# Performance work log

Measured on AMD Instinct MI355X. Metric: run time of the kernel, lower is better.

The kernel has to match this reference:

```python
import jax, jax.numpy as jnp
import numpy as np

EMBED_DIM = 1024
NUM_HEADS = 16
HEAD_DIM = EMBED_DIM // NUM_HEADS  # 64
GRID_H, GRID_W = 24, 24
BASE = 10000.0


def rope2d_cache(head_dim=HEAD_DIM, grid_h=GRID_H, grid_w=GRID_W, base=BASE):
    # "Concatenated Embeddings" 2D RoPE cache -> (cos, sin), each [grid_h*grid_w, head_dim]
    pos_dim = head_dim // 2
    inv_freq = 1.0 / (base ** (jnp.arange(0, pos_dim, 2, dtype=jnp.float32) / pos_dim))
    max_grid = max(grid_h, grid_w)
    positions = jnp.arange(max_grid, dtype=jnp.float32)
    freqs = positions[:, None] * inv_freq[None, :]            # [max_grid, pos_dim//2]
    emb_1d = jnp.concatenate([freqs, freqs], axis=-1)          # [max_grid, pos_dim]
    h_emb = jnp.broadcast_to(emb_1d[:grid_h, None, :], (grid_h, grid_w, pos_dim))
    w_emb = jnp.broadcast_to(emb_1d[None, :grid_w, :], (grid_h, grid_w, pos_dim))
    emb_2d = jnp.concatenate([h_emb, w_emb], axis=-1).reshape(-1, head_dim)
    return jnp.cos(emb_2d), jnp.sin(emb_2d)


def rotate_half(x):
    x1, x2 = jnp.split(x, 2, axis=-1)
    return jnp.concatenate([-x2, x1], axis=-1)


def setup_inputs() -> dict:
    key = jax.random.key(0)
    ks = jax.random.split(key, 9)
    B, S, E = 16, GRID_H * GRID_W + 1, EMBED_DIM
    s = 1.0 / np.sqrt(E)
    inp = {
        "hidden_states": jax.random.normal(ks[0], (B, S, E), dtype=jnp.float32),
        "Wq": jax.random.normal(ks[1], (E, E), dtype=jnp.float32) * s,
        "bq": jnp.zeros((E,), dtype=jnp.float32),
        "Wk": jax.random.normal(ks[2], (E, E), dtype=jnp.float32) * s,
        "bk": jnp.zeros((E,), dtype=jnp.float32),
        "Wv": jax.random.normal(ks[3], (E, E), dtype=jnp.float32) * s,
        "bv": jnp.zeros((E,), dtype=jnp.float32),
        "Wo": jax.random.normal(ks[4], (E, E), dtype=jnp.float32) * s,
        "bo": jnp.zeros((E,), dtype=jnp.float32),
    }
    return inp


def reference(hidden_states, Wq, bq, Wk, bk, Wv, bv, Wo, bo):
    B, S, E = hidden_states.shape
    H, D = NUM_HEADS, HEAD_DIM
    scale = D ** -0.5

    def proj(W, b):
        # torch Linear: x @ W.T + b; reshape to [B, H, S, D]
        y = jnp.einsum('bse,fe->bsf', hidden_states, W) + b
        return y.reshape(B, S, H, D).transpose(0, 2, 1, 3)

    q = proj(Wq, bq)
    k = proj(Wk, bk)
    v = proj(Wv, bv)

    cos, sin = rope2d_cache()                 # [num_patches, D]
    cos = cos[None, None, :, :]
    sin = sin[None, None, :, :]

    # CLS token at position 0 is untouched; RoPE applied to patch tokens 1:
    qp = q[:, :, 1:, :]
    kp = k[:, :, 1:, :]
    qp = qp * cos + rotate_half(qp) * sin
    kp = kp * cos + rotate_half(kp) * sin
    q = jnp.concatenate([q[:, :, :1, :], qp], axis=2)
    k = jnp.concatenate([k[:, :, :1, :], kp], axis=2)

    scores = jnp.einsum('bhqd,bhkd->bhqk', q, k) * scale   # [B,H,S,S]
    attn = jax.nn.softmax(scores, axis=-1)
    out = jnp.einsum('bhqk,bhkd->bhqd', attn, v)           # [B,H,S,D]
    out = out.transpose(0, 2, 1, 3).reshape(B, S, E)
    out = jnp.einsum('bse,fe->bsf', out, Wo) + bo
    return out
```

## Files before the change

### kernel.cpp

```cpp
#include <hip/hip_runtime.h>
#include <hip/hip_bf16.h>
#include <stdint.h>

typedef __bf16 bf16_t;
typedef __attribute__((ext_vector_type(4))) float floatx4;
typedef __attribute__((ext_vector_type(8))) __bf16 bf16x8;
typedef __attribute__((ext_vector_type(4))) __bf16 bf16x4;

#define MFMA16(a, b, c) __builtin_amdgcn_mfma_f32_16x16x32_bf16(a, b, c, 0, 0, 0)

#define GLOAD_LDS16(gsrc, ldst)                                                          \
  __builtin_amdgcn_global_load_lds((const __attribute__((address_space(1))) void*)(gsrc),\
                                   (__attribute__((address_space(3))) void*)(ldst),      \
                                   16, 0, 0)

#define BATCH 16
#define SEQ   577
#define EMB   1024
#define NH    16
#define HD    64
#define SPAD  640
#define MROWS (BATCH * SEQ)
#define MPAD  9344

#define EXP_C 0.1803368801111404f

#define OFF_H  0ULL
#define OFF_WQ 19136512ULL
#define OFF_WK 21233664ULL
#define OFF_WV 23330816ULL
#define OFF_WO 25427968ULL
#define OFF_Q  27525120ULL
#define OFF_K  48496640ULL
#define OFF_VT 69468160ULL
#define OFF_AO 90439680ULL

__global__ __launch_bounds__(256) void k_cast(
    const float4* __restrict__ hs, const float4* __restrict__ wq,
    const float4* __restrict__ wk, const float4* __restrict__ wv,
    const float4* __restrict__ wo, bf16x4* __restrict__ hb, bf16x4* __restrict__ wqb,
    bf16x4* __restrict__ wkb, bf16x4* __restrict__ wvb, bf16x4* __restrict__ wob) {
  int idx = blockIdx.x * 256 + threadIdx.x;
  const int H4 = MROWS * EMB / 4;
  const int W4 = EMB * EMB / 4;
  const float4* src;
  bf16x4* dst;
  int i;
  if (idx < H4) {
    src = hs; dst = hb; i = idx;
  } else {
    int r = idx - H4;
    int w = r / W4;
    if (w >= 4) return;
    i = r - w * W4;
    src = (w == 0) ? wq : (w == 1) ? wk : (w == 2) ? wv : wo;
    dst = (w == 0) ? wqb : (w == 1) ? wkb : (w == 2) ? wvb : wob;
  }
  float4 v = src[i];
  bf16x4 o;
  o.x = (bf16_t)v.x; o.y = (bf16_t)v.y; o.z = (bf16_t)v.z; o.w = (bf16_t)v.w;
  dst[i] = o;
}

__global__ __launch_bounds__(256, 3) void k_qkv(const bf16_t* __restrict__ A,
                                                const bf16_t* __restrict__ Wq,
                                                const bf16_t* __restrict__ Wk,
                                                const bf16_t* __restrict__ Wv,
                                                const float* __restrict__ bq,
                                                const float* __restrict__ bk,
                                                const float* __restrict__ bv,
                                                bf16_t* __restrict__ qb,
                                                bf16_t* __restrict__ kb,
                                                bf16_t* __restrict__ vtb) {
  __shared__ bf16_t As[128 * 32];
  __shared__ bf16_t Bs[3 * 64 * 32];
  const int hh = blockIdx.x;
  const int n0 = hh * 64;
  const int m0 = blockIdx.y * 128;
  const int t = threadIdx.x;
  const int wid = t >> 6, lane = t & 63, quad = lane >> 4, c = lane & 15;

  floatx4 acc[3][2][4];
#pragma unroll
  for (int z = 0; z < 3; z++)
#pragma unroll
    for (int i = 0; i < 2; i++)
#pragma unroll
      for (int j = 0; j < 4; j++) {
        floatx4 zz = {0.f, 0.f, 0.f, 0.f};
        acc[z][i][j] = zz;
      }

  for (int k0 = 0; k0 < EMB; k0 += 32) {
    __syncthreads();
#pragma unroll
    for (int i = 0; i < 2; i++) {
      int ci = i * 256 + t;
      int row = ci >> 2, off = (ci & 3) * 8;
      GLOAD_LDS16(A + (size_t)(m0 + row) * EMB + k0 + off, (char*)As + (i * 256 + wid * 64) * 16);
    }
    {
      int row = t >> 2, off = (t & 3) * 8;
      GLOAD_LDS16(Wq + (size_t)(n0 + row) * EMB + k0 + off, (char*)Bs + (wid * 64) * 16);
      GLOAD_LDS16(Wk + (size_t)(n0 + row) * EMB + k0 + off, (char*)Bs + 4096 + (wid * 64) * 16);
      GLOAD_LDS16(Wv + (size_t)(n0 + row) * EMB + k0 + off, (char*)Bs + 8192 + (wid * 64) * 16);
    }
    __syncthreads();
    bf16x8 af[2];
#pragma unroll
    for (int mi = 0; mi < 2; mi++)
      af[mi] = *(const bf16x8*)(As + (wid * 32 + mi * 16 + c) * 32 + quad * 8);
#pragma unroll
    for (int z = 0; z < 3; z++) {
      bf16x8 bfr[4];
#pragma unroll
      for (int ni = 0; ni < 4; ni++)
        bfr[ni] = *(const bf16x8*)(Bs + z * 2048 + (ni * 16 + c) * 32 + quad * 8);
#pragma unroll
      for (int mi = 0; mi < 2; mi++)
#pragma unroll
        for (int ni = 0; ni < 4; ni++) acc[z][mi][ni] = MFMA16(af[mi], bfr[ni], acc[z][mi][ni]);
    }
  }

  const float invf = exp2f(-(float)c * 0.8304820237218405f);

  for (int z = 0; z < 3; z++) {
    const float* bias = (z == 0) ? bq : (z == 1) ? bk : bv;
    float bias_v[4];
#pragma unroll
    for (int ni = 0; ni < 4; ni++) bias_v[ni] = bias[n0 + ni * 16 + c];
#pragma unroll
    for (int mi = 0; mi < 2; mi++) {
#pragma unroll
      for (int r = 0; r < 4; r++) {
        int m = m0 + wid * 32 + mi * 16 + quad * 4 + r;
        if (m >= MROWS) continue;
        int bb = m / SEQ;
        int s = m - bb * SEQ;
        if (z < 2) {
          float ch = 1.f, sh = 0.f, cw = 1.f, sw = 0.f;
          if (s > 0) {
            int p = s - 1;
            int hp = p / 24, wp = p - (p / 24) * 24;
            __sincosf((float)hp * invf, &sh, &ch);
            __sincosf((float)wp * invf, &sw, &cw);
          }
          bf16_t* dst = (z == 0) ? qb : kb;
          size_t rowoff = ((size_t)(bb * NH + hh) * SPAD + s) * HD;
#pragma unroll
          for (int ni = 0; ni < 4; ni++) {
            float val = acc[z][mi][ni][r] + bias_v[ni];
            float part = acc[z][mi][ni ^ 2][r] + bias_v[ni ^ 2];
            float rot = (ni < 2) ? -part : part;
            float cs = (ni < 2) ? ch : cw;
            float sn = (ni < 2) ? sh : sw;
            dst[rowoff + ni * 16 + c] = (bf16_t)(val * cs + rot * sn);
          }
        } else {
          size_t base = (size_t)(bb * NH + hh) * HD;
#pragma unroll
          for (int ni = 0; ni < 4; ni++) {
            float val = acc[z][mi][ni][r] + bias_v[ni];
            int d = ni * 16 + c;
            vtb[(base + d) * SPAD + s] = (bf16_t)val;
          }
        }
      }
    }
  }
}

#define PSTR 72
#define OSTR 66
__global__ __launch_bounds__(256, 4) void k_attn(const bf16_t* __restrict__ qb,
                                                 const bf16_t* __restrict__ kb,
                                                 const bf16_t* __restrict__ vtb,
                                                 bf16_t* __restrict__ ao) {
  __shared__ __align__(16) bf16_t smem[13824];
  bf16_t* Ks = smem;
  bf16_t* Vs = smem + 4608;
  bf16_t* Ps = smem + 9216;
  const int t = threadIdx.x, wid = t >> 6, lane = t & 63, quad = lane >> 4, c = lane & 15;
  const int hh = blockIdx.x, bb = blockIdx.y, qt = blockIdx.z;
  const size_t bh = (size_t)bb * NH + hh;
  const bf16_t* qbase = qb + bh * SPAD * HD + (size_t)qt * 128 * HD;
  const bf16_t* kbase = kb + bh * SPAD * HD;
  const bf16_t* vbase = vtb + bh * HD * SPAD;
  bf16_t* Pw = Ps + wid * 1152;

  bf16x8 aq[2][2];
#pragma unroll
  for (int mi = 0; mi < 2; mi++)
#pragma unroll
    for (int h = 0; h < 2; h++)
      aq[mi][h] = *(const bf16x8*)(qbase + (size_t)(wid * 32 + mi * 16 + c) * HD + h * 32 + quad * 8);

  uint4 kr[2], vr[2];
#pragma unroll
  for (int j = 0; j < 2; j++) {
    int ci = j * 256 + t;
    int row = ci >> 3, off = (ci & 7) * 8;
    kr[j] = *(const uint4*)(kbase + (size_t)row * HD + off);
    vr[j] = *(const uint4*)(vbase + (size_t)row * SPAD + off);
  }

  bf16x8 ones;
#pragma unroll
  for (int i = 0; i < 8; i++) ones[i] = (bf16_t)1.0f;

  floatx4 acc_o[2][4], acc_l[2];
#pragma unroll
  for (int mi = 0; mi < 2; mi++) {
    floatx4 z = {0.f, 0.f, 0.f, 0.f};
    acc_l[mi] = z;
#pragma unroll
    for (int nd = 0; nd < 4; nd++) acc_o[mi][nd] = z;
  }

  for (int kt = 0; kt < 9; kt++) {
    __syncthreads();
#pragma unroll
    for (int j = 0; j < 2; j++) {
      int ci = j * 256 + t;
      int row = ci >> 3, off = (ci & 7) * 8;
      *(uint4*)((char*)Ks + (row * PSTR + off) * 2) = kr[j];
      *(uint4*)((char*)Vs + (row * PSTR + off) * 2) = vr[j];
    }
    __syncthreads();
    if (kt < 8) {
#pragma unroll
      for (int j = 0; j < 2; j++) {
        int ci = j * 256 + t;
        int row = ci >> 3, off = (ci & 7) * 8;
        kr[j] = *(const uint4*)(kbase + (size_t)((kt + 1) * 64 + row) * HD + off);
        vr[j] = *(const uint4*)(vbase + (size_t)row * SPAD + (kt + 1) * 64 + off);
      }
    }

    floatx4 sc[2][4];
#pragma unroll
    for (int ni = 0; ni < 4; ni++) {
      bf16x8 k0 = *(const bf16x8*)(Ks + (ni * 16 + c) * PSTR + quad * 8);
      bf16x8 k1 = *(const bf16x8*)(Ks + (ni * 16 + c) * PSTR + 32 + quad * 8);
#pragma unroll
      for (int mi = 0; mi < 2; mi++) {
        floatx4 zz = {0.f, 0.f, 0.f, 0.f};
        zz = MFMA16(aq[mi][0], k0, zz);
        zz = MFMA16(aq[mi][1], k1, zz);
        sc[mi][ni] = zz;
      }
    }

#pragma unroll
    for (int mi = 0; mi < 2; mi++) {
#pragma unroll
      for (int ni = 0; ni < 4; ni++)
#pragma unroll
        for (int r = 0; r < 4; r++) {
          float p = exp2f(sc[mi][ni][r] * EXP_C);
          Pw[(quad * 4 + r) * PSTR + ni * 16 + c] = (bf16_t)p;
        }
      bf16x8 pa0 = *(const bf16x8*)(Pw + c * PSTR + quad * 8);
      bf16x8 pa1 = *(const bf16x8*)(Pw + c * PSTR + 32 + quad * 8);
#pragma unroll
      for (int nd = 0; nd < 4; nd++) {
        bf16x8 v0 = *(const bf16x8*)(Vs + (nd * 16 + c) * PSTR + quad * 8);
        bf16x8 v1 = *(const bf16x8*)(Vs + (nd * 16 + c) * PSTR + 32 + quad * 8);
        acc_o[mi][nd] = MFMA16(pa0, v0, acc_o[mi][nd]);
        acc_o[mi][nd] = MFMA16(pa1, v1, acc_o[mi][nd]);
      }
      acc_l[mi] = MFMA16(pa0, ones, acc_l[mi]);
      acc_l[mi] = MFMA16(pa1, ones, acc_l[mi]);
    }
  }

  {
    bf16x8 klast[2];
#pragma unroll
    for (int h = 0; h < 2; h++) {
      bf16x8 kk;
#pragma unroll
      for (int i = 0; i < 8; i++) kk[i] = (bf16_t)0.0f;
      if (c == 0) kk = *(const bf16x8*)(kbase + (size_t)576 * HD + h * 32 + quad * 8);
      klast[h] = kk;
    }
    float vlast[4];
#pragma unroll
    for (int nd = 0; nd < 4; nd++)
      vlast[nd] = (float)vbase[(size_t)(nd * 16 + c) * SPAD + 576];
#pragma unroll
    for (int mi = 0; mi < 2; mi++) {
      floatx4 zz = {0.f, 0.f, 0.f, 0.f};
      zz = MFMA16(aq[mi][0], klast[0], zz);
      zz = MFMA16(aq[mi][1], klast[1], zz);
#pragma unroll
      for (int r = 0; r < 4; r++) {
        float p = exp2f(zz[r] * EXP_C);
        p = __shfl(p, quad * 16, 64);
#pragma unroll
        for (int nd = 0; nd < 4; nd++) acc_o[mi][nd][r] += p * vlast[nd];
        acc_l[mi][r] += p;
      }
    }
  }

  {
    const int rsub = lane >> 3, c8 = lane & 7;
#pragma unroll
    for (int mi = 0; mi < 2; mi++) {
#pragma unroll
      for (int r = 0; r < 4; r++) {
        float inv_l = 1.f / acc_l[mi][r];
        int row = quad * 4 + r;
#pragma unroll
        for (int nd = 0; nd < 4; nd++)
          Pw[row * OSTR + nd * 16 + c] = (bf16_t)(acc_o[mi][nd][r] * inv_l);
      }
#pragma unroll
      for (int j = 0; j < 2; j++) {
        int row = j * 8 + rsub;
        bf16x8 ov = *(const bf16x8*)(Pw + row * OSTR + c8 * 8);
        int q = qt * 128 + wid * 32 + mi * 16 + row;
        if (q < SEQ) {
          size_t mrow = (size_t)bb * SEQ + q;
          *(bf16x8*)(ao + mrow * EMB + hh * HD + c8 * 8) = ov;
        }
      }
    }
  }
}

__global__ __launch_bounds__(256) void k_oproj(const bf16_t* __restrict__ A,
                                               const bf16_t* __restrict__ Wo,
                                               const float* __restrict__ bo,
                                               float* __restrict__ out) {
  __shared__ bf16_t As[128 * 32];
  __shared__ bf16_t Bs[128 * 32];
  const int n0 = blockIdx.x * 128, m0 = blockIdx.y * 128;
  const int t = threadIdx.x;
  const int wid = t >> 6, lane = t & 63, quad = lane >> 4, c = lane & 15;
  const int wr = wid >> 1, wc = wid & 1;
  floatx4 acc[4][4];
#pragma unroll
  for (int i = 0; i < 4; i++)
#pragma unroll
    for (int j = 0; j < 4; j++) {
      floatx4 z = {0.f, 0.f, 0.f, 0.f};
      acc[i][j] = z;
    }
  for (int k0 = 0; k0 < EMB; k0 += 32) {
    __syncthreads();
#pragma unroll
    for (int i = 0; i < 2; i++) {
      int ci = i * 256 + t;
      int row = ci >> 2, off = (ci & 3) * 8;
      GLOAD_LDS16(A + (size_t)(m0 + row) * EMB + k0 + off, (char*)As + (i * 256 + wid * 64) * 16);
      GLOAD_LDS16(Wo + (size_t)(n0 + row) * EMB + k0 + off, (char*)Bs + (i * 256 + wid * 64) * 16);
    }
    __syncthreads();
    bf16x8 af[4], bfr[4];
#pragma unroll
    for (int mi = 0; mi < 4; mi++)
      af[mi] = *(const bf16x8*)(As + (wr * 64 + mi * 16 + c) * 32 + quad * 8);
#pragma unroll
    for (int ni = 0; ni < 4; ni++)
      bfr[ni] = *(const bf16x8*)(Bs + (wc * 64 + ni * 16 + c) * 32 + quad * 8);
#pragma unroll
    for (int mi = 0; mi < 4; mi++)
#pragma unroll
      for (int ni = 0; ni < 4; ni++) acc[mi][ni] = MFMA16(af[mi], bfr[ni], acc[mi][ni]);
  }
  float bias_v[4];
#pragma unroll
  for (int ni = 0; ni < 4; ni++) bias_v[ni] = bo[n0 + wc * 64 + ni * 16 + c];
#pragma unroll
  for (int mi = 0; mi < 4; mi++)
#pragma unroll
    for (int r = 0; r < 4; r++) {
      int m = m0 + wr * 64 + mi * 16 + quad * 4 + r;
      if (m >= MROWS) continue;
#pragma unroll
      for (int ni = 0; ni < 4; ni++)
        out[(size_t)m * EMB + n0 + wc * 64 + ni * 16 + c] = acc[mi][ni][r] + bias_v[ni];
    }
}

extern "C" void kernel_launch(void* const* d_in, const int* in_sizes, int n_in, void* d_out,
                              int out_size, void* d_ws, size_t ws_size, hipStream_t stream) {
  const float* hs = (const float*)d_in[0];
  const float* Wq = (const float*)d_in[1];
  const float* bq = (const float*)d_in[2];
  const float* Wk = (const float*)d_in[3];
  const float* bk = (const float*)d_in[4];
  const float* Wv = (const float*)d_in[5];
  const float* bv = (const float*)d_in[6];
  const float* Wo = (const float*)d_in[7];
  const float* bo = (const float*)d_in[8];
  float* out = (float*)d_out;
  char* ws = (char*)d_ws;

  bf16_t* hb = (bf16_t*)(ws + OFF_H);
  bf16_t* wqb = (bf16_t*)(ws + OFF_WQ);
  bf16_t* wkb = (bf16_t*)(ws + OFF_WK);
  bf16_t* wvb = (bf16_t*)(ws + OFF_WV);
  bf16_t* wob = (bf16_t*)(ws + OFF_WO);
  bf16_t* qbuf = (bf16_t*)(ws + OFF_Q);
  bf16_t* kbuf = (bf16_t*)(ws + OFF_K);
  bf16_t* vtbuf = (bf16_t*)(ws + OFF_VT);
  bf16_t* aob = (bf16_t*)(ws + OFF_AO);


  k_cast<<<13328, 256, 0, stream>>>((const float4*)hs, (const float4*)Wq, (const float4*)Wk,
                                    (const float4*)Wv, (const float4*)Wo, (bf16x4*)hb,
                                    (bf16x4*)wqb, (bf16x4*)wkb, (bf16x4*)wvb, (bf16x4*)wob);

  dim3 gq(16, 73);
  k_qkv<<<gq, 256, 0, stream>>>(hb, wqb, wkb, wvb, bq, bk, bv, qbuf, kbuf, vtbuf);

  dim3 ga(16, 16, 5);
  k_attn<<<ga, 256, 0, stream>>>(qbuf, kbuf, vtbuf, aob);

  dim3 go(8, 73);
  k_oproj<<<go, 256, 0, stream>>>(aob, wob, bo, out);
}
```

Measured before the change: 328.8 us.

## Double-buffer LDS tiles in QKV and output projection GEMM loops

Both projection GEMM kernels now keep two LDS stages and issue the async global-to-LDS loads for the next K tile before computing on the current one. There is one barrier per iteration instead of two. The aim is to hide global load latency behind the MFMA work. In exchange, LDS use per block doubles, which may cut occupancy. The compiler may also still insert conservative vmcnt waits that serialize the loads.

```diff
diff --git a/kernel.cpp b/kernel.cpp
--- a/kernel.cpp
+++ b/kernel.cpp
@@ -72,14 +72,31 @@
                                                 bf16_t* __restrict__ qb,
                                                 bf16_t* __restrict__ kb,
                                                 bf16_t* __restrict__ vtb) {
-  __shared__ bf16_t As[128 * 32];
-  __shared__ bf16_t Bs[3 * 64 * 32];
+  __shared__ __align__(16) bf16_t smem[2 * 10240];
   const int hh = blockIdx.x;
   const int n0 = hh * 64;
   const int m0 = blockIdx.y * 128;
   const int t = threadIdx.x;
   const int wid = t >> 6, lane = t & 63, quad = lane >> 4, c = lane & 15;
 
+  const int arow0 = t >> 2, aoff = (t & 3) * 8;
+  const int arow1 = 64 + arow0;
+  const int brow = t >> 2, boff = (t & 3) * 8;
+
+#define QKV_STAGE(buf, k0)                                                                  \
+  {                                                                                         \
+    bf16_t* As_ = smem + (buf) * 10240;                                                     \
+    bf16_t* Bs_ = As_ + 4096;                                                               \
+    GLOAD_LDS16(A + (size_t)(m0 + arow0) * EMB + (k0) + aoff, (char*)As_ + (wid * 64) * 16);\
+    GLOAD_LDS16(A + (size_t)(m0 + arow1) * EMB + (k0) + aoff,                               \
+                (char*)As_ + (256 + wid * 64) * 16);                                        \
+    GLOAD_LDS16(Wq + (size_t)(n0 + brow) * EMB + (k0) + boff, (char*)Bs_ + (wid * 64) * 16);\
+    GLOAD_LDS16(Wk + (size_t)(n0 + brow) * EMB + (k0) + boff,                               \
+                (char*)Bs_ + 4096 + (wid * 64) * 16);                                       \
+    GLOAD_LDS16(Wv + (size_t)(n0 + brow) * EMB + (k0) + boff,                               \
+                (char*)Bs_ + 8192 + (wid * 64) * 16);                                       \
+  }
+
   floatx4 acc[3][2][4];
 #pragma unroll
   for (int z = 0; z < 3; z++)
@@ -91,37 +108,32 @@
         acc[z][i][j] = zz;
       }
 
-  for (int k0 = 0; k0 < EMB; k0 += 32) {
-    __syncthreads();
-#pragma unroll
-    for (int i = 0; i < 2; i++) {
-      int ci = i * 256 + t;
-      int row = ci >> 2, off = (ci & 3) * 8;
-      GLOAD_LDS16(A + (size_t)(m0 + row) * EMB + k0 + off, (char*)As + (i * 256 + wid * 64) * 16);
-    }
-    {
-      int row = t >> 2, off = (t & 3) * 8;
-      GLOAD_LDS16(Wq + (size_t)(n0 + row) * EMB + k0 + off, (char*)Bs + (wid * 64) * 16);
-      GLOAD_LDS16(Wk + (size_t)(n0 + row) * EMB + k0 + off, (char*)Bs + 4096 + (wid * 64) * 16);
-      GLOAD_LDS16(Wv + (size_t)(n0 + row) * EMB + k0 + off, (char*)Bs + 8192 + (wid * 64) * 16);
-    }
-    __syncthreads();
+  QKV_STAGE(0, 0);
+  __syncthreads();
+  int cur = 0;
+  for (int kt = 0; kt < 32; kt++) {
+    if (kt < 31) QKV_STAGE(cur ^ 1, (kt + 1) * 32);
+    const bf16_t* Asc = smem + cur * 10240;
+    const bf16_t* Bsc = Asc + 4096;
     bf16x8 af[2];
 #pragma unroll
     for (int mi = 0; mi < 2; mi++)
-      af[mi] = *(const bf16x8*)(As + (wid * 32 + mi * 16 + c) * 32 + quad * 8);
+      af[mi] = *(const bf16x8*)(Asc + (wid * 32 + mi * 16 + c) * 32 + quad * 8);
 #pragma unroll
     for (int z = 0; z < 3; z++) {
       bf16x8 bfr[4];
 #pragma unroll
       for (int ni = 0; ni < 4; ni++)
-        bfr[ni] = *(const bf16x8*)(Bs + z * 2048 + (ni * 16 + c) * 32 + quad * 8);
+        bfr[ni] = *(const bf16x8*)(Bsc + z * 2048 + (ni * 16 + c) * 32 + quad * 8);
 #pragma unroll
       for (int mi = 0; mi < 2; mi++)
 #pragma unroll
         for (int ni = 0; ni < 4; ni++) acc[z][mi][ni] = MFMA16(af[mi], bfr[ni], acc[z][mi][ni]);
     }
-  }
+    __syncthreads();
+    cur ^= 1;
+  }
+#undef QKV_STAGE
 
   const float invf = exp2f(-(float)c * 0.8304820237218405f);
 
@@ -335,12 +347,26 @@
                                                const bf16_t* __restrict__ Wo,
                                                const float* __restrict__ bo,
                                                float* __restrict__ out) {
-  __shared__ bf16_t As[128 * 32];
-  __shared__ bf16_t Bs[128 * 32];
+  __shared__ __align__(16) bf16_t smem[2 * 8192];
   const int n0 = blockIdx.x * 128, m0 = blockIdx.y * 128;
   const int t = threadIdx.x;
   const int wid = t >> 6, lane = t & 63, quad = lane >> 4, c = lane & 15;
   const int wr = wid >> 1, wc = wid & 1;
+  const int row0 = t >> 2, off0 = (t & 3) * 8;
+  const int row1 = 64 + row0;
+
+#define OPROJ_STAGE(buf, k0)                                                                 \
+  {                                                                                          \
+    bf16_t* As_ = smem + (buf) * 8192;                                                       \
+    bf16_t* Bs_ = As_ + 4096;                                                                \
+    GLOAD_LDS16(A + (size_t)(m0 + row0) * EMB + (k0) + off0, (char*)As_ + (wid * 64) * 16);  \
+    GLOAD_LDS16(A + (size_t)(m0 + row1) * EMB + (k0) + off0,                                 \
+                (char*)As_ + (256 + wid * 64) * 16);                                         \
+    GLOAD_LDS16(Wo + (size_t)(n0 + row0) * EMB + (k0) + off0, (char*)Bs_ + (wid * 64) * 16); \
+    GLOAD_LDS16(Wo + (size_t)(n0 + row1) * EMB + (k0) + off0,                                \
+                (char*)Bs_ + (256 + wid * 64) * 16);                                         \
+  }
+
   floatx4 acc[4][4];
 #pragma unroll
   for (int i = 0; i < 4; i++)
@@ -349,28 +375,30 @@
       floatx4 z = {0.f, 0.f, 0.f, 0.f};
       acc[i][j] = z;
     }
-  for (int k0 = 0; k0 < EMB; k0 += 32) {
+
+  OPROJ_STAGE(0, 0);
+  __syncthreads();
+  int cur = 0;
+  for (int kt = 0; kt < 32; kt++) {
+    if (kt < 31) OPROJ_STAGE(cur ^ 1, (kt + 1) * 32);
+    const bf16_t* Asc = smem + cur * 8192;
+    const bf16_t* Bsc = Asc + 4096;
+    bf16x8 af[4], bfr[4];
+#pragma unroll
+    for (int mi = 0; mi < 4; mi++)
+      af[mi] = *(const bf16x8*)(Asc + (wr * 64 + mi * 16 + c) * 32 + quad * 8);
+#pragma unroll
+    for (int ni = 0; ni < 4; ni++)
+      bfr[ni] = *(const bf16x8*)(Bsc + (wc * 64 + ni * 16 + c) * 32 + quad * 8);
+#pragma unroll
+    for (int mi = 0; mi < 4; mi++)
+#pragma unroll
+      for (int ni = 0; ni < 4; ni++) acc[mi][ni] = MFMA16(af[mi], bfr[ni], acc[mi][ni]);
     __syncthreads();
-#pragma unroll
-    for (int i = 0; i < 2; i++) {
-      int ci = i * 256 + t;
-      int row = ci >> 2, off = (ci & 3) * 8;
-      GLOAD_LDS16(A + (size_t)(m0 + row) * EMB + k0 + off, (char*)As + (i * 256 + wid * 64) * 16);
-      GLOAD_LDS16(Wo + (size_t)(n0 + row) * EMB + k0 + off, (char*)Bs + (i * 256 + wid * 64) * 16);
-    }
-    __syncthreads();
-    bf16x8 af[4], bfr[4];
-#pragma unroll
-    for (int mi = 0; mi < 4; mi++)
-      af[mi] = *(const bf16x8*)(As + (wr * 64 + mi * 16 + c) * 32 + quad * 8);
-#pragma unroll
-    for (int ni = 0; ni < 4; ni++)
-      bfr[ni] = *(const bf16x8*)(Bs + (wc * 64 + ni * 16 + c) * 32 + quad * 8);
-#pragma unroll
-    for (int mi = 0; mi < 4; mi++)
-#pragma unroll
-      for (int ni = 0; ni < 4; ni++) acc[mi][ni] = MFMA16(af[mi], bfr[ni], acc[mi][ni]);
-  }
+    cur ^= 1;
+  }
+#undef OPROJ_STAGE
+
   float bias_v[4];
 #pragma unroll
   for (int ni = 0; ni < 4; ni++) bias_v[ni] = bo[n0 + wc * 64 + ni * 16 + c];
```

New measurement: 324.2 us. About the same (-1.4%).

## Load GEMM operands directly from global into registers, dropping LDS staging

Applied to the files above, without the earlier changes.

The QKV and output-projection GEMMs stop staging A and W tiles through shared memory with barriers. Each wave now loads its MFMA fragments straight from global memory into registers, relying on L1/L2 caching for reuse across waves. This removes LDS traffic and the per-iteration __syncthreads, but it multiplies global/L2 load requests, since the weight tile is re-read by every wave, and leaves no software prefetch. The attention kernel's occupancy hint is also raised from 4 to 5 blocks and k_oproj gets a min-blocks hint of 3.

```diff
diff --git a/kernel.cpp b/kernel.cpp
--- a/kernel.cpp
+++ b/kernel.cpp
@@ -8,11 +8,6 @@
 typedef __attribute__((ext_vector_type(4))) __bf16 bf16x4;
 
 #define MFMA16(a, b, c) __builtin_amdgcn_mfma_f32_16x16x32_bf16(a, b, c, 0, 0, 0)
-
-#define GLOAD_LDS16(gsrc, ldst)                                                          \
-  __builtin_amdgcn_global_load_lds((const __attribute__((address_space(1))) void*)(gsrc),\
-                                   (__attribute__((address_space(3))) void*)(ldst),      \
-                                   16, 0, 0)
 
 #define BATCH 16
 #define SEQ   577
@@ -72,8 +67,6 @@
                                                 bf16_t* __restrict__ qb,
                                                 bf16_t* __restrict__ kb,
                                                 bf16_t* __restrict__ vtb) {
-  __shared__ bf16_t As[128 * 32];
-  __shared__ bf16_t Bs[3 * 64 * 32];
   const int hh = blockIdx.x;
   const int n0 = hh * 64;
   const int m0 = blockIdx.y * 128;
@@ -91,35 +84,30 @@
         acc[z][i][j] = zz;
       }
 
+  const bf16_t* ap0 = A + (size_t)(m0 + wid * 32 + c) * EMB + quad * 8;
+  const bf16_t* ap1 = ap0 + (size_t)16 * EMB;
+  const bf16_t* wp[3];
+  wp[0] = Wq + (size_t)(n0 + c) * EMB + quad * 8;
+  wp[1] = Wk + (size_t)(n0 + c) * EMB + quad * 8;
+  wp[2] = Wv + (size_t)(n0 + c) * EMB + quad * 8;
+
   for (int k0 = 0; k0 < EMB; k0 += 32) {
-    __syncthreads();
-#pragma unroll
-    for (int i = 0; i < 2; i++) {
-      int ci = i * 256 + t;
-      int row = ci >> 2, off = (ci & 3) * 8;
-      GLOAD_LDS16(A + (size_t)(m0 + row) * EMB + k0 + off, (char*)As + (i * 256 + wid * 64) * 16);
-    }
-    {
-      int row = t >> 2, off = (t & 3) * 8;
-      GLOAD_LDS16(Wq + (size_t)(n0 + row) * EMB + k0 + off, (char*)Bs + (wid * 64) * 16);
-      GLOAD_LDS16(Wk + (size_t)(n0 + row) * EMB + k0 + off, (char*)Bs + 4096 + (wid * 64) * 16);
-      GLOAD_LDS16(Wv + (size_t)(n0 + row) * EMB + k0 + off, (char*)Bs + 8192 + (wid * 64) * 16);
-    }
-    __syncthreads();
-    bf16x8 af[2];
-#pragma unroll
-    for (int mi = 0; mi < 2; mi++)
-      af[mi] = *(const bf16x8*)(As + (wid * 32 + mi * 16 + c) * 32 + quad * 8);
+    bf16x8 af0 = *(const bf16x8*)(ap0 + k0);
+    bf16x8 af1 = *(const bf16x8*)(ap1 + k0);
 #pragma unroll
     for (int z = 0; z < 3; z++) {
-      bf16x8 bfr[4];
-#pragma unroll
-      for (int ni = 0; ni < 4; ni++)
-        bfr[ni] = *(const bf16x8*)(Bs + z * 2048 + (ni * 16 + c) * 32 + quad * 8);
-#pragma unroll
-      for (int mi = 0; mi < 2; mi++)
-#pragma unroll
-        for (int ni = 0; ni < 4; ni++) acc[z][mi][ni] = MFMA16(af[mi], bfr[ni], acc[z][mi][ni]);
+      bf16x8 b0 = *(const bf16x8*)(wp[z] + k0);
+      bf16x8 b1 = *(const bf16x8*)(wp[z] + (size_t)16 * EMB + k0);
+      bf16x8 b2 = *(const bf16x8*)(wp[z] + (size_t)32 * EMB + k0);
+      bf16x8 b3 = *(const bf16x8*)(wp[z] + (size_t)48 * EMB + k0);
+      acc[z][0][0] = MFMA16(af0, b0, acc[z][0][0]);
+      acc[z][1][0] = MFMA16(af1, b0, acc[z][1][0]);
+      acc[z][0][1] = MFMA16(af0, b1, acc[z][0][1]);
+      acc[z][1][1] = MFMA16(af1, b1, acc[z][1][1]);
+      acc[z][0][2] = MFMA16(af0, b2, acc[z][0][2]);
+      acc[z][1][2] = MFMA16(af1, b2, acc[z][1][2]);
+      acc[z][0][3] = MFMA16(af0, b3, acc[z][0][3]);
+      acc[z][1][3] = MFMA16(af1, b3, acc[z][1][3]);
     }
   }
 
@@ -142,9 +130,9 @@
           float ch = 1.f, sh = 0.f, cw = 1.f, sw = 0.f;
           if (s > 0) {
             int p = s - 1;
-            int hp = p / 24, wp = p - (p / 24) * 24;
+            int hp = p / 24, wp2 = p - (p / 24) * 24;
             __sincosf((float)hp * invf, &sh, &ch);
-            __sincosf((float)wp * invf, &sw, &cw);
+            __sincosf((float)wp2 * invf, &sw, &cw);
           }
           bf16_t* dst = (z == 0) ? qb : kb;
           size_t rowoff = ((size_t)(bb * NH + hh) * SPAD + s) * HD;
@@ -173,7 +161,7 @@
 
 #define PSTR 72
 #define OSTR 66
-__global__ __launch_bounds__(256, 4) void k_attn(const bf16_t* __restrict__ qb,
+__global__ __launch_bounds__(256, 5) void k_attn(const bf16_t* __restrict__ qb,
                                                  const bf16_t* __restrict__ kb,
                                                  const bf16_t* __restrict__ vtb,
                                                  bf16_t* __restrict__ ao) {
@@ -331,16 +319,15 @@
   }
 }
 
-__global__ __launch_bounds__(256) void k_oproj(const bf16_t* __restrict__ A,
-                                               const bf16_t* __restrict__ Wo,
-                                               const float* __restrict__ bo,
-                                               float* __restrict__ out) {
-  __shared__ bf16_t As[128 * 32];
-  __shared__ bf16_t Bs[128 * 32];
+__global__ __launch_bounds__(256, 3) void k_oproj(const bf16_t* __restrict__ A,
+                                                  const bf16_t* __restrict__ Wo,
+                                                  const float* __restrict__ bo,
+                                                  float* __restrict__ out) {
   const int n0 = blockIdx.x * 128, m0 = blockIdx.y * 128;
   const int t = threadIdx.x;
   const int wid = t >> 6, lane = t & 63, quad = lane >> 4, c = lane & 15;
   const int wr = wid >> 1, wc = wid & 1;
+
   floatx4 acc[4][4];
 #pragma unroll
   for (int i = 0; i < 4; i++)
@@ -349,28 +336,24 @@
       floatx4 z = {0.f, 0.f, 0.f, 0.f};
       acc[i][j] = z;
     }
+
+  const bf16_t* ap = A + (size_t)(m0 + wr * 64 + c) * EMB + quad * 8;
+  const bf16_t* bp = Wo + (size_t)(n0 + wc * 64 + c) * EMB + quad * 8;
+
   for (int k0 = 0; k0 < EMB; k0 += 32) {
-    __syncthreads();
-#pragma unroll
-    for (int i = 0; i < 2; i++) {
-      int ci = i * 256 + t;
-      int row = ci >> 2, off = (ci & 3) * 8;
-      GLOAD_LDS16(A + (size_t)(m0 + row) * EMB + k0 + off, (char*)As + (i * 256 + wid * 64) * 16);
-      GLOAD_LDS16(Wo + (size_t)(n0 + row) * EMB + k0 + off, (char*)Bs + (i * 256 + wid * 64) * 16);
-    }
-    __syncthreads();
     bf16x8 af[4], bfr[4];
 #pragma unroll
     for (int mi = 0; mi < 4; mi++)
-      af[mi] = *(const bf16x8*)(As + (wr * 64 + mi * 16 + c) * 32 + quad * 8);
+      af[mi] = *(const bf16x8*)(ap + (size_t)mi * 16 * EMB + k0);
 #pragma unroll
     for (int ni = 0; ni < 4; ni++)
-      bfr[ni] = *(const bf16x8*)(Bs + (wc * 64 + ni * 16 + c) * 32 + quad * 8);
+      bfr[ni] = *(const bf16x8*)(bp + (size_t)ni * 16 * EMB + k0);
 #pragma unroll
     for (int mi = 0; mi < 4; mi++)
 #pragma unroll
       for (int ni = 0; ni < 4; ni++) acc[mi][ni] = MFMA16(af[mi], bfr[ni], acc[mi][ni]);
   }
+
   float bias_v[4];
 #pragma unroll
   for (int ni = 0; ni < 4; ni++) bias_v[ni] = bo[n0 + wc * 64 + ni * 16 + c];
```

Result: slower. 666.6 us (+102.8%).
